# Kernel tuning notes

Measured on AMD Instinct MI355X. Metric: run time of the kernel, lower is better.

Reference implementation:

```python
import jax, jax.numpy as jnp
import numpy as np

B, S, A, H, DH, DM = 4, 4096, 2, 8, 128, 2048


def setup_inputs() -> dict:
    key = jax.random.key(0)
    k_x, k_i, k_p, k_w, k_b = jax.random.split(key, 5)
    embedding = jax.random.normal(k_x, (B, S, A, DH), dtype=jnp.float32)
    sel_idx = jax.random.randint(k_i, (B, S, A), 0, H)
    probs = jax.random.uniform(k_p, (B, S, A), dtype=jnp.float32)
    sel_probs = probs / jnp.sum(probs, axis=-1, keepdims=True)  # valid head probabilities
    W = jax.random.normal(k_w, (H, DH, DM), dtype=jnp.float32) * 0.02  # per-head weight banks
    b = jax.random.normal(k_b, (H, DM), dtype=jnp.float32) * 0.02      # per-head biases
    return {"embedding": embedding, "sel_idx": sel_idx, "sel_probs": sel_probs, "W": W, "b": b}


def reference(embedding, sel_idx, sel_probs, W, b):
    # BankedLinear with squeeze=True: out = sum_a p_a * (x_a @ W[idx_a] + b[idx_a])
    # Route prob-weighted inputs into head buckets via one-hot (avoids materializing
    # gathered [T, A, DH, DM] weights), then one dense GEMM per head bank.
    onehot = jax.nn.one_hot(sel_idx, H, dtype=embedding.dtype)           # (B,S,A,H)
    xw = embedding * sel_probs[..., None]                                 # (B,S,A,DH)
    routed = jnp.einsum('bsad,bsah->bshd', xw, onehot)                    # (B,S,H,DH)
    y = jnp.einsum('bshd,hdm->bsm', routed, W)                            # (B,S,DM)
    y = y + jnp.einsum('bsah,hm->bsm', onehot * sel_probs[..., None], b)  # weighted bias
    return y
```

## Files before the change

### kernel.cpp

```cpp
#include <hip/hip_runtime.h>
#include <hip/hip_bf16.h>

#define T_TOK 16384
#define NH 8
#define DHD 128
#define DMD 2048
#define KTOT 256
#define BCAP 384
#define CSTR 64

typedef __attribute__((ext_vector_type(8))) short bf16x8;
typedef __attribute__((ext_vector_type(4))) float f32x4;

__device__ inline short f2b(float x) {
    __hip_bfloat16 h = __float2bfloat16(x);
    return *reinterpret_cast<short*>(&h);
}

__device__ inline void gll16(const void* g, void* l) {
    __builtin_amdgcn_global_load_lds(
        (const __attribute__((address_space(1))) void*)g,
        (__attribute__((address_space(3))) void*)l, 16, 0, 0);
}


__global__ __launch_bounds__(1024) void k_init(int* __restrict__ cursor) {
    cursor[blockIdx.x * 1024 + threadIdx.x] = 0;
}

__global__ __launch_bounds__(256) void k_work(
    const int* __restrict__ idx, const float* __restrict__ emb,
    const float* __restrict__ probs, const float* __restrict__ W,
    int* __restrict__ cursor, int* __restrict__ perm,
    short* __restrict__ Apk, short* __restrict__ Wt) {
    if (blockIdx.x < 512) {
        int g = blockIdx.x * 256 + threadIdx.x;
        int t = g >> 3, sub = g & 7;
        int lane = threadIdx.x & 63;
        int pos = 0;
        if (sub == 0) {
            int key = idx[2 * t] * NH + idx[2 * t + 1];
            int slot = atomicAdd(&cursor[key * CSTR], 1);
            pos = (slot < BCAP) ? (key * BCAP + slot) : -1;
            if (pos >= 0) perm[pos] = t;
        }
        pos = __shfl(pos, lane & ~7, 64);
        if (pos < 0) return;
        int a = sub >> 2;
        float p = probs[2 * t + a];
        const f32x4* s =
            (const f32x4*)(emb + ((size_t)(2 * t + a)) * DHD + (sub & 3) * 32);
        short* dst = Apk + (size_t)pos * KTOT + sub * 32;
#pragma unroll
        for (int c = 0; c < 4; ++c) {
            f32x4 f0 = s[2 * c], f1 = s[2 * c + 1];
            bf16x8 o;
            o[0] = f2b(p * f0.x); o[1] = f2b(p * f0.y);
            o[2] = f2b(p * f0.z); o[3] = f2b(p * f0.w);
            o[4] = f2b(p * f1.x); o[5] = f2b(p * f1.y);
            o[6] = f2b(p * f1.z); o[7] = f2b(p * f1.w);
            *(bf16x8*)(dst + c * 8) = o;
        }
    } else {
        __shared__ float Ws[DHD][65];
        int bx = blockIdx.x - 512;
        int h = bx >> 5, m0 = (bx & 31) * 64;
        int tid = threadIdx.x;
        for (int i = tid; i < DHD * 64; i += 256) {
            int d = i >> 6, m = i & 63;
            Ws[d][m] = W[((size_t)h * DHD + d) * DMD + m0 + m];
        }
        __syncthreads();
        for (int i = tid; i < 64 * 16; i += 256) {
            int m = i >> 4, d0 = (i & 15) * 8;
            bf16x8 o;
#pragma unroll
            for (int j = 0; j < 8; ++j) o[j] = f2b(Ws[d0 + j][m]);
            *(bf16x8*)(Wt + ((size_t)h * DMD + m0 + m) * DHD + d0) = o;
        }
    }
}

__global__ __launch_bounds__(512) void k_gemm(
    const short* __restrict__ Apk, const float* __restrict__ probs,
    const short* __restrict__ Wt, const float* __restrict__ bias,
    const int* __restrict__ perm, const int* __restrict__ cursor,
    float* __restrict__ out) {
    int lin  = blockIdx.x;
    int work = (lin & 7) * 192 + (lin >> 3);
    int tile_id = work >> 3;
    int ncol    = (work & 7) * 256;
    int key = tile_id / 3, s = tile_id - key * 3;
    int nrows = cursor[key * CSTR] - s * 128;
    if (nrows <= 0) return;
    if (nrows > 128) nrows = 128;
    int row0 = key * BCAP + s * 128;
    int h0 = key >> 3, h1 = key & 7;

    __shared__ short As[128 * 64];
    __shared__ short Bs[256 * 64];
    __shared__ int   s_tok[128];
    __shared__ float s_p0[128], s_p1[128];

    int tid = threadIdx.x;
    int lane = tid & 63, wave = tid >> 6;

    if (tid < 128) {
        int t = -1; float p0 = 0.f, p1 = 0.f;
        if (tid < nrows) {
            t = perm[row0 + tid];
            p0 = probs[2 * t];
            p1 = probs[2 * t + 1];
        }
        s_tok[tid] = t; s_p0[tid] = p0; s_p1[tid] = p1;
    }

    f32x4 acc[4][4];
#pragma unroll
    for (int i = 0; i < 4; ++i)
#pragma unroll
        for (int j = 0; j < 4; ++j) acc[i][j] = (f32x4){0.f, 0.f, 0.f, 0.f};

    int wm = (wave >> 2) * 64;
    int wn = (wave & 3) * 64;
    int l15 = lane & 15, lq = lane >> 4;

    int srcr = tid >> 3;
    int cs   = (tid & 7) ^ (srcr & 7);

    for (int ks = 0; ks < 4; ++ks) {
        int h     = (ks < 2) ? h0 : h1;
        int kg0   = ks * 64;
        int dbase = (ks & 1) * 64;
#pragma unroll
        for (int rd = 0; rd < 2; ++rd) {
            int r = rd * 64 + srcr;
            short* ldst = As + (rd * 512 + wave * 64) * 8;
            gll16(Apk + (size_t)(row0 + r) * KTOT + kg0 + cs * 8, ldst);
        }
#pragma unroll
        for (int rd = 0; rd < 4; ++rd) {
            int r = rd * 64 + srcr;
            short* ldst = Bs + (rd * 512 + wave * 64) * 8;
            gll16(Wt + ((size_t)h * DMD + ncol + r) * DHD + dbase + cs * 8, ldst);
        }
        __syncthreads();

#pragma unroll
        for (int ki = 0; ki < 2; ++ki) {
            bf16x8 af[4], bfr[4];
#pragma unroll
            for (int mi = 0; mi < 4; ++mi) {
                int R  = wm + mi * 16 + l15;
                int ch = (ki * 4 + lq) ^ (R & 7);
                af[mi] = *(const bf16x8*)&As[R * 64 + ch * 8];
            }
#pragma unroll
            for (int ni = 0; ni < 4; ++ni) {
                int N  = wn + ni * 16 + l15;
                int ch = (ki * 4 + lq) ^ (N & 7);
                bfr[ni] = *(const bf16x8*)&Bs[N * 64 + ch * 8];
            }
#pragma unroll
            for (int mi = 0; mi < 4; ++mi)
#pragma unroll
                for (int ni = 0; ni < 4; ++ni)
                    acc[mi][ni] = __builtin_amdgcn_mfma_f32_16x16x32_bf16(
                        af[mi], bfr[ni], acc[mi][ni], 0, 0, 0);
        }
        __syncthreads();
    }

#pragma unroll
    for (int ni = 0; ni < 4; ++ni) {
        int c = ncol + wn + ni * 16 + l15;
        float b0 = bias[h0 * DMD + c];
        float b1 = bias[h1 * DMD + c];
#pragma unroll
        for (int mi = 0; mi < 4; ++mi) {
#pragma unroll
            for (int r = 0; r < 4; ++r) {
                int i = wm + mi * 16 + lq * 4 + r;
                int t = s_tok[i];
                if (t >= 0) {
                    float v = acc[mi][ni][r] + s_p0[i] * b0 + s_p1[i] * b1;
                    __builtin_nontemporal_store(v, &out[(size_t)t * DMD + c]);
                }
            }
        }
    }
}

extern "C" void kernel_launch(void* const* d_in, const int* in_sizes, int n_in,
                              void* d_out, int out_size, void* d_ws, size_t ws_size,
                              hipStream_t stream) {
    const float* emb      = (const float*)d_in[0];
    const int*   sel_idx  = (const int*)d_in[1];
    const float* sel_prob = (const float*)d_in[2];
    const float* W        = (const float*)d_in[3];
    const float* bias     = (const float*)d_in[4];
    float* out = (float*)d_out;

    char* ws = (char*)d_ws;
    int* cursor = (int*)(ws + 0);
    int* perm   = (int*)(ws + 16384);
    short* Wt   = (short*)(ws + 262144);
    short* Apk  = (short*)(ws + 4456448);

    k_init<<<dim3(4), dim3(1024), 0, stream>>>(cursor);
    k_work<<<dim3(768), dim3(256), 0, stream>>>(
        sel_idx, emb, sel_prob, W, cursor, perm, Apk, Wt);
    k_gemm<<<dim3(1536), dim3(512), 0, stream>>>(
        Apk, sel_prob, Wt, bias, perm, cursor, out);
}
```

Measured before the change: 75.67 us.

## Double-buffer GEMM LDS tiles with async loads overlapping MFMA compute

Splits the K loop of the routed GEMM into eight 32-wide stages with two LDS buffers. The next stage's global_load_lds is issued while the current stage's MFMAs run, synchronised with explicit vmcnt waits and barriers. The aim is to hide global memory latency that previously stalled each of the four 64-wide K steps. The cost is more barriers, a new swizzle pattern, and reliance on hand-counted vmcnt values being correct.

```diff
diff --git a/kernel.cpp b/kernel.cpp
--- a/kernel.cpp
+++ b/kernel.cpp
@@ -97,8 +97,8 @@
     int row0 = key * BCAP + s * 128;
     int h0 = key >> 3, h1 = key & 7;
 
-    __shared__ short As[128 * 64];
-    __shared__ short Bs[256 * 64];
+    __shared__ short As[2][128 * 32];
+    __shared__ short Bs[2][256 * 32];
     __shared__ int   s_tok[128];
     __shared__ float s_p0[128], s_p1[128];
 
@@ -114,6 +114,7 @@
         }
         s_tok[tid] = t; s_p0[tid] = p0; s_p1[tid] = p1;
     }
+    __syncthreads();
 
     f32x4 acc[4][4];
 #pragma unroll
@@ -125,51 +126,56 @@
     int wn = (wave & 3) * 64;
     int l15 = lane & 15, lq = lane >> 4;
 
-    int srcr = tid >> 3;
-    int cs   = (tid & 7) ^ (srcr & 7);
-
-    for (int ks = 0; ks < 4; ++ks) {
-        int h     = (ks < 2) ? h0 : h1;
-        int kg0   = ks * 64;
-        int dbase = (ks & 1) * 64;
-#pragma unroll
-        for (int rd = 0; rd < 2; ++rd) {
-            int r = rd * 64 + srcr;
-            short* ldst = As + (rd * 512 + wave * 64) * 8;
-            gll16(Apk + (size_t)(row0 + r) * KTOT + kg0 + cs * 8, ldst);
-        }
-#pragma unroll
-        for (int rd = 0; rd < 4; ++rd) {
-            int r = rd * 64 + srcr;
-            short* ldst = Bs + (rd * 512 + wave * 64) * 8;
-            gll16(Wt + ((size_t)h * DMD + ncol + r) * DHD + dbase + cs * 8, ldst);
-        }
-        __syncthreads();
-
-#pragma unroll
-        for (int ki = 0; ki < 2; ++ki) {
-            bf16x8 af[4], bfr[4];
-#pragma unroll
-            for (int mi = 0; mi < 4; ++mi) {
-                int R  = wm + mi * 16 + l15;
-                int ch = (ki * 4 + lq) ^ (R & 7);
-                af[mi] = *(const bf16x8*)&As[R * 64 + ch * 8];
-            }
-#pragma unroll
-            for (int ni = 0; ni < 4; ++ni) {
-                int N  = wn + ni * 16 + l15;
-                int ch = (ki * 4 + lq) ^ (N & 7);
-                bfr[ni] = *(const bf16x8*)&Bs[N * 64 + ch * 8];
-            }
-#pragma unroll
-            for (int mi = 0; mi < 4; ++mi)
-#pragma unroll
-                for (int ni = 0; ni < 4; ++ni)
-                    acc[mi][ni] = __builtin_amdgcn_mfma_f32_16x16x32_bf16(
-                        af[mi], bfr[ni], acc[mi][ni], 0, 0, 0);
-        }
-        __syncthreads();
-    }
+    int arow = tid >> 2;
+    int clog = (tid & 3) ^ ((tid >> 3) & 3);
+
+    auto stage = [&](int ks, int p) {
+        int h = (ks < 4) ? h0 : h1;
+        const short* asrc =
+            Apk + (size_t)(row0 + arow) * KTOT + (ks << 5) + clog * 8;
+        const short* bbase =
+            Wt + ((size_t)h * DMD + ncol) * DHD + ((ks & 3) << 5) + clog * 8;
+        gll16(asrc, &As[p][wave * 512]);
+        gll16(bbase + (size_t)arow * DHD, &Bs[p][wave * 512]);
+        gll16(bbase + (size_t)(arow + 128) * DHD, &Bs[p][wave * 512 + 4096]);
+    };
+
+    auto compute = [&](int p) {
+        bf16x8 af[4], bfr[4];
+#pragma unroll
+        for (int mi = 0; mi < 4; ++mi) {
+            int R  = wm + mi * 16 + l15;
+            int ph = lq ^ ((R >> 1) & 3);
+            af[mi] = *(const bf16x8*)&As[p][R * 32 + ph * 8];
+        }
+#pragma unroll
+        for (int ni = 0; ni < 4; ++ni) {
+            int N  = wn + ni * 16 + l15;
+            int ph = lq ^ ((N >> 1) & 3);
+            bfr[ni] = *(const bf16x8*)&Bs[p][N * 32 + ph * 8];
+        }
+#pragma unroll
+        for (int mi = 0; mi < 4; ++mi)
+#pragma unroll
+            for (int ni = 0; ni < 4; ++ni)
+                acc[mi][ni] = __builtin_amdgcn_mfma_f32_16x16x32_bf16(
+                    af[mi], bfr[ni], acc[mi][ni], 0, 0, 0);
+    };
+
+    stage(0, 0);
+    stage(1, 1);
+#define STEP(S, NW)                                                  \
+    asm volatile("s_waitcnt vmcnt(" #NW ")" ::: "memory");           \
+    __builtin_amdgcn_s_barrier();                                    \
+    __builtin_amdgcn_sched_barrier(0);                               \
+    compute(S & 1);                                                  \
+    __builtin_amdgcn_sched_barrier(0);                               \
+    __builtin_amdgcn_s_barrier();                                    \
+    __builtin_amdgcn_sched_barrier(0);                               \
+    if (S + 2 < 8) stage(S + 2, S & 1);
+    STEP(0, 3) STEP(1, 3) STEP(2, 3) STEP(3, 3)
+    STEP(4, 3) STEP(5, 3) STEP(6, 3) STEP(7, 0)
+#undef STEP
 
 #pragma unroll
     for (int ni = 0; ni < 4; ++ni) {
```

New measurement: 78.59 us. 1.04x slower.
